# Performance work log

Measured on AMD Instinct MI355X. Metric: run time of the kernel, lower is better.

## Reference

```python
import jax, jax.numpy as jnp
import numpy as np

VERTEX_W = 1.0
SMOOTH_W = 0.1
SYM_W = 0.05
CHAMFER_W = 0.1

B, N = 4, 8192  # N points per cloud, flat dim = N*3


def setup_inputs() -> dict:
    key = jax.random.key(0)
    k1, k2 = jax.random.split(key)
    pred = jax.random.normal(k1, (B, N * 3), dtype=jnp.float32)
    targ = jax.random.normal(k2, (B, N * 3), dtype=jnp.float32)
    return {"pred_vertices": pred, "target_vertices": targ}


def _chamfer(x, y):
    # x: [B,N,3], y: [B,M,3]; euclidean cdist via matmul expansion
    x2 = jnp.sum(x * x, axis=-1)  # [B,N]
    y2 = jnp.sum(y * y, axis=-1)  # [B,M]
    xy = jnp.einsum('bnd,bmd->bnm', x, y)  # [B,N,M]
    d2 = x2[:, :, None] + y2[None if False else slice(None), None, :] - 2.0 * xy
    d = jnp.sqrt(jnp.maximum(d2, 0.0))
    return jnp.mean(jnp.min(d, axis=2)) + jnp.mean(jnp.min(d, axis=1))


def reference(pred_vertices, target_vertices):
    b = pred_vertices.shape[0]
    pv = pred_vertices.reshape(b, -1, 3)
    tv = target_vertices.reshape(b, -1, 3)

    # vertex MSE (on flat tensors, same as mse on reshaped)
    vertex_loss = jnp.mean((pred_vertices - target_vertices) ** 2)

    # smoothness: mean L2 norm of consecutive vertex diffs
    diff = pv[:, 1:, :] - pv[:, :-1, :]
    smoothness_loss = jnp.mean(jnp.linalg.norm(diff, axis=2))

    # symmetry: N is even in this config
    mid = pv.shape[1] // 2
    left = pv[:, :mid, :]
    right = jnp.flip(pv[:, mid:, :], axis=1)
    right = right.at[:, :, 0].multiply(-1.0)
    symmetry_loss = jnp.mean((left - right) ** 2)

    chamfer_loss = _chamfer(pv, tv)

    total = (VERTEX_W * vertex_loss + SMOOTH_W * smoothness_loss
             + SYM_W * symmetry_loss + CHAMFER_W * chamfer_loss)
    return total
```

## Files before the change

kernel.cpp:

```cpp
#include <hip/hip_runtime.h>
#include <hip/hip_bf16.h>


#define B_ 4
#define N_ 8192
#define MID_ (N_ / 2)
#define CNT_OFF 1536
#define RP_OFF 1664
#define PM_OFF 4096
#define PMC_OFF (PM_OFF + 8 * B_ * N_)
#define PACK_OFF (PMC_OFF + 16 * B_ * N_)
#define PACK_STRIDE (B_ * N_ * 16)

typedef short short8 __attribute__((ext_vector_type(8)));
typedef float f32x16 __attribute__((ext_vector_type(16)));

__global__ void AdvancedLoss3D_1881195675843_kernel() {}

__device__ __forceinline__ void async16(void* lds, const void* g) {
    __builtin_amdgcn_global_load_lds(
        (const __attribute__((address_space(1))) unsigned int*)g,
        (__attribute__((address_space(3))) unsigned int*)lds,
        16, 0, 0);
}

__device__ inline unsigned short bfu(float x) {
    union { __hip_bfloat16 b; unsigned short u; } c;
    c.b = __float2bfloat16(x);
    return c.u;
}
__device__ inline float bff(unsigned short u) {
    union { __hip_bfloat16 b; unsigned short u; } c;
    c.u = u;
    return __bfloat162float(c.b);
}

__device__ __forceinline__ float min3f(float a, float b, float c) {
    return fminf(fminf(a, b), c);
}
__device__ __forceinline__ float tree16(f32x16 v) {
    float m0 = min3f(v[0],  v[1],  v[2]);
    float m1 = min3f(v[3],  v[4],  v[5]);
    float m2 = min3f(v[6],  v[7],  v[8]);
    float m3 = min3f(v[9],  v[10], v[11]);
    float m4 = min3f(v[12], v[13], v[14]);
    return fminf(min3f(m0, m1, m2), min3f(m3, m4, v[15]));
}

__device__ inline void encA(float x, float y, float z, unsigned short* A) {
    float n2 = fmaf(x, x, fmaf(y, y, z * z));
    unsigned short hx = bfu(x), hy = bfu(y), hz = bfu(z);
    float fx = bff(hx), fy = bff(hy), fz = bff(hz);
    unsigned short lx = bfu(x - fx), ly = bfu(y - fy), lz = bfu(z - fz);
    unsigned short mx = bfu(-2.f * fx), my = bfu(-2.f * fy), mz = bfu(-2.f * fz);
    unsigned short nx = bfu(-2.f * bff(lx)), ny = bfu(-2.f * bff(ly)),
                   nz = bfu(-2.f * bff(lz));
    unsigned short n2h = bfu(n2);
    unsigned short n2l = bfu(n2 - bff(n2h));
    unsigned short one = bfu(1.0f);
    A[0] = mx; A[1] = my; A[2] = mz;
    A[3] = mx; A[4] = my; A[5] = mz;
    A[6] = nx; A[7] = ny; A[8] = nz;
    A[9] = n2h; A[10] = n2l; A[11] = one; A[12] = one;
    A[13] = A[14] = A[15] = 0;
}
__device__ inline void encB(float x, float y, float z, unsigned short* Bv) {
    float n2 = fmaf(x, x, fmaf(y, y, z * z));
    unsigned short hx = bfu(x), hy = bfu(y), hz = bfu(z);
    float fx = bff(hx), fy = bff(hy), fz = bff(hz);
    unsigned short lx = bfu(x - fx), ly = bfu(y - fy), lz = bfu(z - fz);
    unsigned short n2h = bfu(n2);
    unsigned short n2l = bfu(n2 - bff(n2h));
    unsigned short one = bfu(1.0f);
    Bv[0] = hx; Bv[1] = hy; Bv[2] = hz;
    Bv[3] = lx; Bv[4] = ly; Bv[5] = lz;
    Bv[6] = hx; Bv[7] = hy; Bv[8] = hz;
    Bv[9] = one; Bv[10] = one; Bv[11] = n2h; Bv[12] = n2l;
    Bv[13] = Bv[14] = Bv[15] = 0;
}

__global__ __launch_bounds__(64) void prep_aux(const float* __restrict__ pred,
                                               const float* __restrict__ targ,
                                               float* __restrict__ ws) {
    int idx = blockIdx.x * 64 + threadIdx.x;
    int b = idx >> 13;
    int i = idx & (N_ - 1);
    const float* p = pred + (size_t)idx * 3;
    const float* t = targ + (size_t)idx * 3;
    float px = p[0], py = p[1], pz = p[2];
    float tx = t[0], ty = t[1], tz = t[2];

    if (idx == 0) ((unsigned int*)ws)[CNT_OFF] = 0u;

    unsigned short* pk = (unsigned short*)(ws + PACK_OFF);
    {
        union U { unsigned short s[16]; uint4 q[2]; } ua, ud;
        encA(px, py, pz, ua.s);
        encB(tx, ty, tz, ud.s);
        uint4* ap = (uint4*)(pk + (size_t)idx * 16);
        ap[0] = ua.q[0]; ap[1] = ua.q[1];
        uint4* bt = (uint4*)(pk + PACK_STRIDE + (size_t)idx * 16);
        bt[0] = ud.q[0]; bt[1] = ud.q[1];
    }

    float dx = px - tx, dy = py - ty, dz = pz - tz;
    float dv = dx * dx + dy * dy + dz * dz;

    float sm = 0.f;
    if (i < N_ - 1) {
        float ex = p[3] - px, ey = p[4] - py, ez = p[5] - pz;
        sm = sqrtf(ex * ex + ey * ey + ez * ez);
    }

    float sy = 0.f;
    if (i < MID_) {
        const float* r = pred + ((size_t)(b * N_ + (N_ - 1 - i))) * 3;
        float ax = px + r[0];
        float ay = py - r[1];
        float az = pz - r[2];
        sy = ax * ax + ay * ay + az * az;
    }

    for (int off = 32; off; off >>= 1) {
        dv += __shfl_down(dv, off, 64);
        sm += __shfl_down(sm, off, 64);
        sy += __shfl_down(sy, off, 64);
    }
    if (threadIdx.x == 0) {
        ws[3 * blockIdx.x + 0] = dv;
        ws[3 * blockIdx.x + 1] = sm;
        ws[3 * blockIdx.x + 2] = sy;
    }
}

__global__ __launch_bounds__(256, 2) void chamfer_mfma(const unsigned short* __restrict__ packs,
                                                       float* __restrict__ ws) {
    int bid = blockIdx.x;
    int chunk = bid & 31;
    int rgb = bid >> 5;
    int b   = chunk >> 3;
    int cc  = chunk & 7;
    int w   = threadIdx.x >> 6;
    int l   = threadIdx.x & 63;
    int lr  = l & 31;
    int kh  = l >> 5;

    const unsigned short* Ap = packs;
    const unsigned short* Bp = packs + PACK_STRIDE;

    int rowbase = (rgb * 4 + w) * 128;
    const unsigned short* abase = Ap + ((size_t)(b * N_ + rowbase + lr)) * 16 + kh * 8;
    short8 af[4];
#pragma unroll
    for (int i = 0; i < 4; i++)
        af[i] = *(const short8*)(abase + i * 32 * 16);

    float rmin[4][16];
#pragma unroll
    for (int i = 0; i < 4; i++)
#pragma unroll
        for (int j = 0; j < 16; j++) rmin[i][j] = 3.4e38f;

    __shared__ __align__(16) unsigned char smem[65536];
    float (*colbuf)[1024] = (float (*)[1024])(smem + 32768);

    const unsigned short* bchunk = Bp + (size_t)(b * N_ + cc * 1024) * 16;
    {
        const unsigned short* src = bchunk + (size_t)(lr * 16 + kh * 8);
#pragma unroll
        for (int t = 0; t < 8; t++) {
            int tile = w * 8 + t;
            async16(smem + (size_t)tile * 1024, src + (size_t)tile * 512);
        }
    }
    __syncthreads();

    const f32x16 zero = {0.f, 0.f, 0.f, 0.f, 0.f, 0.f, 0.f, 0.f,
                         0.f, 0.f, 0.f, 0.f, 0.f, 0.f, 0.f, 0.f};
    const unsigned char* bl = smem + kh * 512 + lr * 16;
    for (int t = 0; t < 32; t += 2) {
        short8 bE = *(const short8*)(bl + (size_t)t * 1024);
        short8 bO = *(const short8*)(bl + (size_t)(t + 1) * 1024);
        float cmE = 3.4e38f, cmO = 3.4e38f;
#pragma unroll
        for (int i = 0; i < 4; i++) {
            f32x16 aE = __builtin_amdgcn_mfma_f32_32x32x16_bf16(af[i], bE, zero, 0, 0, 0);
            f32x16 aO = __builtin_amdgcn_mfma_f32_32x32x16_bf16(af[i], bO, zero, 0, 0, 0);
#pragma unroll
            for (int j = 0; j < 16; j++)
                rmin[i][j] = min3f(rmin[i][j], aE[j], aO[j]);
            cmE = fminf(cmE, tree16(aE));
            cmO = fminf(cmO, tree16(aO));
        }
        cmE = fminf(cmE, __shfl_xor(cmE, 32, 64));
        cmO = fminf(cmO, __shfl_xor(cmO, 32, 64));
        colbuf[w][t * 32 + lr] = cmE;
        colbuf[w][(t + 1) * 32 + lr] = cmO;
    }
    __syncthreads();

    {
        float* pmc = ws + PMC_OFF + (size_t)rgb * 32768 + b * N_ + cc * 1024;
#pragma unroll
        for (int c0 = 0; c0 < 1024; c0 += 256) {
            int c = c0 + threadIdx.x;
            pmc[c] = fminf(fminf(colbuf[0][c], colbuf[1][c]),
                           fminf(colbuf[2][c], colbuf[3][c]));
        }
    }
    __syncthreads();

    float (*sred)[128][32] = (float (*)[128][32])smem;
#pragma unroll
    for (int i = 0; i < 4; i++)
#pragma unroll
        for (int j = 0; j < 16; j++) {
            int r = i * 32 + (j & 3) + 8 * (j >> 2) + 4 * kh;
            sred[w][r][(lr + r) & 31] = rmin[i][j];
        }
    __syncthreads();
    float* orow = ws + PM_OFF + (size_t)cc * 32768 + b * N_ + rowbase;
#pragma unroll
    for (int rr = 0; rr < 128; rr += 64) {
        int r = rr + l;
        float v = 3.4e38f;
#pragma unroll
        for (int c = 0; c < 32; c++)
            v = fminf(v, sred[w][r][(c + r) & 31]);
        orow[r] = v;
    }
}

__global__ __launch_bounds__(256) void reduce_compose(const float* __restrict__ ws_ro,
                                                      float* __restrict__ ws,
                                                      unsigned int* __restrict__ out) {
    int bid = blockIdx.x, tid = threadIdx.x;
    int idx = bid * 256 + tid;
    float v = 3.4e38f;
    if (idx < B_ * N_) {
        const float* pmr = ws_ro + PM_OFF;
#pragma unroll
        for (int s = 0; s < 8; s++)
            v = fminf(v, pmr[(size_t)s * 32768 + idx]);
    } else {
        int c = idx - B_ * N_;
        const float* pmc = ws_ro + PMC_OFF;
#pragma unroll
        for (int s = 0; s < 16; s++)
            v = fminf(v, pmc[(size_t)s * 32768 + c]);
    }
    float d = sqrtf(fmaxf(v, 0.f));
    for (int off = 32; off; off >>= 1) d += __shfl_down(d, off, 64);
    __shared__ float red[4];
    __shared__ int is_last;
    int lane = tid & 63, w = tid >> 6;
    if (lane == 0) red[w] = d;
    __syncthreads();
    if (tid == 0) {
        ws[RP_OFF + bid] = red[0] + red[1] + red[2] + red[3];
        __threadfence();
        unsigned old = atomicAdd((unsigned int*)ws + CNT_OFF, 1u);
        is_last = (old == 255u);
    }
    __syncthreads();
    if (!is_last) return;

    if (tid == 0) __threadfence();
    __syncthreads();
    float rp = ws[RP_OFF + tid];
    float cr = (tid < 128) ? rp : 0.f;
    float cc = (tid < 128) ? 0.f : rp;
    float dv = ws[3 * tid]     + ws[3 * (tid + 256)];
    float sm = ws[3 * tid + 1] + ws[3 * (tid + 256) + 1];
    float sy = ws[3 * tid + 2] + ws[3 * (tid + 256) + 2];
    for (int off = 32; off; off >>= 1) {
        dv += __shfl_down(dv, off, 64);
        sm += __shfl_down(sm, off, 64);
        sy += __shfl_down(sy, off, 64);
        cr += __shfl_down(cr, off, 64);
        cc += __shfl_down(cc, off, 64);
    }
    __shared__ float red5[5][4];
    if (lane == 0) { red5[0][w] = dv; red5[1][w] = sm; red5[2][w] = sy;
                     red5[3][w] = cr; red5[4][w] = cc; }
    __syncthreads();
    if (tid == 0) {
        float S[5];
#pragma unroll
        for (int q = 0; q < 5; q++)
            S[q] = red5[q][0] + red5[q][1] + red5[q][2] + red5[q][3];
        float vertex = S[0] / (float)(B_ * N_ * 3);
        float smooth = S[1] / (float)(B_ * (N_ - 1));
        float sym    = S[2] / (float)(B_ * MID_ * 3);
        float cham   = (S[3] + S[4]) / (float)(B_ * N_);
        float total  = vertex + 0.1f * smooth + 0.05f * sym + 0.1f * cham;
        union { __hip_bfloat16 b; unsigned short u; } cv;
        cv.b = __float2bfloat16(total);
        out[0] = ((unsigned int)cv.u << 16) | (unsigned int)cv.u;
    }
}

extern "C" void kernel_launch(void* const* d_in, const int* in_sizes, int n_in,
                              void* d_out, int out_size, void* d_ws, size_t ws_size,
                              hipStream_t stream) {
    (void)in_sizes; (void)n_in; (void)out_size; (void)ws_size;
    const float* pred = (const float*)d_in[0];
    const float* targ = (const float*)d_in[1];
    float* wsf = (float*)d_ws;

    prep_aux<<<dim3(512), dim3(64), 0, stream>>>(pred, targ, wsf);
    chamfer_mfma<<<dim3(512), dim3(256), 0, stream>>>(
        (const unsigned short*)(wsf + PACK_OFF), wsf);
    reduce_compose<<<dim3(256), dim3(256), 0, stream>>>(
        wsf, wsf, (unsigned int*)d_out);
}
```

Before: 83.20 us.

## Fuse bf16 encoding into chamfer kernel and move aux losses into reduction

Result: faster. 79.16 us, median of 2 (-4.8%).

```diff
diff --git a/kernel.cpp b/kernel.cpp
--- a/kernel.cpp
+++ b/kernel.cpp
@@ -9,20 +9,11 @@
 #define RP_OFF 1664
 #define PM_OFF 4096
 #define PMC_OFF (PM_OFF + 8 * B_ * N_)
-#define PACK_OFF (PMC_OFF + 16 * B_ * N_)
-#define PACK_STRIDE (B_ * N_ * 16)
 
 typedef short short8 __attribute__((ext_vector_type(8)));
 typedef float f32x16 __attribute__((ext_vector_type(16)));
 
 __global__ void AdvancedLoss3D_1881195675843_kernel() {}
-
-__device__ __forceinline__ void async16(void* lds, const void* g) {
-    __builtin_amdgcn_global_load_lds(
-        (const __attribute__((address_space(1))) unsigned int*)g,
-        (__attribute__((address_space(3))) unsigned int*)lds,
-        16, 0, 0);
-}
 
 __device__ inline unsigned short bfu(float x) {
     union { __hip_bfloat16 b; unsigned short u; } c;
@@ -47,7 +38,7 @@
     return fminf(min3f(m0, m1, m2), min3f(m3, m4, v[15]));
 }
 
-__device__ inline void encA(float x, float y, float z, unsigned short* A) {
+__device__ __forceinline__ short8 encA_half(float x, float y, float z, int kh) {
     float n2 = fmaf(x, x, fmaf(y, y, z * z));
     unsigned short hx = bfu(x), hy = bfu(y), hz = bfu(z);
     float fx = bff(hx), fy = bff(hy), fz = bff(hz);
@@ -58,13 +49,14 @@
     unsigned short n2h = bfu(n2);
     unsigned short n2l = bfu(n2 - bff(n2h));
     unsigned short one = bfu(1.0f);
-    A[0] = mx; A[1] = my; A[2] = mz;
-    A[3] = mx; A[4] = my; A[5] = mz;
-    A[6] = nx; A[7] = ny; A[8] = nz;
-    A[9] = n2h; A[10] = n2l; A[11] = one; A[12] = one;
-    A[13] = A[14] = A[15] = 0;
-}
-__device__ inline void encB(float x, float y, float z, unsigned short* Bv) {
+    short8 lo = {(short)mx, (short)my, (short)mz, (short)mx,
+                 (short)my, (short)mz, (short)nx, (short)ny};
+    short8 hi = {(short)nz, (short)n2h, (short)n2l, (short)one,
+                 (short)one, 0, 0, 0};
+    return kh ? hi : lo;
+}
+__device__ __forceinline__ void encB(float x, float y, float z,
+                                     unsigned short* Bv) {
     float n2 = fmaf(x, x, fmaf(y, y, z * z));
     unsigned short hx = bfu(x), hy = bfu(y), hz = bfu(z);
     float fx = bff(hx), fy = bff(hy), fz = bff(hz);
@@ -79,100 +71,55 @@
     Bv[13] = Bv[14] = Bv[15] = 0;
 }
 
-__global__ __launch_bounds__(64) void prep_aux(const float* __restrict__ pred,
-                                               const float* __restrict__ targ,
-                                               float* __restrict__ ws) {
-    int idx = blockIdx.x * 64 + threadIdx.x;
-    int b = idx >> 13;
-    int i = idx & (N_ - 1);
-    const float* p = pred + (size_t)idx * 3;
-    const float* t = targ + (size_t)idx * 3;
-    float px = p[0], py = p[1], pz = p[2];
-    float tx = t[0], ty = t[1], tz = t[2];
-
-    if (idx == 0) ((unsigned int*)ws)[CNT_OFF] = 0u;
-
-    unsigned short* pk = (unsigned short*)(ws + PACK_OFF);
-    {
-        union U { unsigned short s[16]; uint4 q[2]; } ua, ud;
-        encA(px, py, pz, ua.s);
-        encB(tx, ty, tz, ud.s);
-        uint4* ap = (uint4*)(pk + (size_t)idx * 16);
-        ap[0] = ua.q[0]; ap[1] = ua.q[1];
-        uint4* bt = (uint4*)(pk + PACK_STRIDE + (size_t)idx * 16);
-        bt[0] = ud.q[0]; bt[1] = ud.q[1];
-    }
-
-    float dx = px - tx, dy = py - ty, dz = pz - tz;
-    float dv = dx * dx + dy * dy + dz * dz;
-
-    float sm = 0.f;
-    if (i < N_ - 1) {
-        float ex = p[3] - px, ey = p[4] - py, ez = p[5] - pz;
-        sm = sqrtf(ex * ex + ey * ey + ez * ez);
-    }
-
-    float sy = 0.f;
-    if (i < MID_) {
-        const float* r = pred + ((size_t)(b * N_ + (N_ - 1 - i))) * 3;
-        float ax = px + r[0];
-        float ay = py - r[1];
-        float az = pz - r[2];
-        sy = ax * ax + ay * ay + az * az;
-    }
-
-    for (int off = 32; off; off >>= 1) {
-        dv += __shfl_down(dv, off, 64);
-        sm += __shfl_down(sm, off, 64);
-        sy += __shfl_down(sy, off, 64);
-    }
-    if (threadIdx.x == 0) {
-        ws[3 * blockIdx.x + 0] = dv;
-        ws[3 * blockIdx.x + 1] = sm;
-        ws[3 * blockIdx.x + 2] = sy;
-    }
-}
-
-__global__ __launch_bounds__(256, 2) void chamfer_mfma(const unsigned short* __restrict__ packs,
+__global__ __launch_bounds__(256, 2) void chamfer_mfma(const float* __restrict__ pred,
+                                                       const float* __restrict__ targ,
                                                        float* __restrict__ ws) {
     int bid = blockIdx.x;
     int chunk = bid & 31;
     int rgb = bid >> 5;
     int b   = chunk >> 3;
     int cc  = chunk & 7;
-    int w   = threadIdx.x >> 6;
-    int l   = threadIdx.x & 63;
+    int tid = threadIdx.x;
+    int w   = tid >> 6;
+    int l   = tid & 63;
     int lr  = l & 31;
     int kh  = l >> 5;
 
-    const unsigned short* Ap = packs;
-    const unsigned short* Bp = packs + PACK_STRIDE;
-
-    int rowbase = (rgb * 4 + w) * 128;
-    const unsigned short* abase = Ap + ((size_t)(b * N_ + rowbase + lr)) * 16 + kh * 8;
-    short8 af[4];
-#pragma unroll
-    for (int i = 0; i < 4; i++)
-        af[i] = *(const short8*)(abase + i * 32 * 16);
-
-    float rmin[4][16];
-#pragma unroll
-    for (int i = 0; i < 4; i++)
-#pragma unroll
-        for (int j = 0; j < 16; j++) rmin[i][j] = 3.4e38f;
+    if (bid == 0 && tid == 0)
+        ((unsigned int*)ws)[CNT_OFF] = 0u;
 
     __shared__ __align__(16) unsigned char smem[65536];
     float (*colbuf)[1024] = (float (*)[1024])(smem + 32768);
 
-    const unsigned short* bchunk = Bp + (size_t)(b * N_ + cc * 1024) * 16;
     {
-        const unsigned short* src = bchunk + (size_t)(lr * 16 + kh * 8);
-#pragma unroll
-        for (int t = 0; t < 8; t++) {
-            int tile = w * 8 + t;
-            async16(smem + (size_t)tile * 1024, src + (size_t)tile * 512);
-        }
-    }
+        const float* tb = targ + (size_t)(b * N_ + cc * 1024) * 3;
+#pragma unroll
+        for (int j = 0; j < 4; j++) {
+            int c = tid + 256 * j;
+            float x = tb[3 * c], y = tb[3 * c + 1], z = tb[3 * c + 2];
+            union { unsigned short s[16]; uint4 q[2]; } e;
+            encB(x, y, z, e.s);
+            unsigned char* base = smem + (size_t)(c >> 5) * 1024 + (c & 31) * 16;
+            *(uint4*)(base)       = e.q[0];
+            *(uint4*)(base + 512) = e.q[1];
+        }
+    }
+
+    int rowbase = (rgb * 4 + w) * 128;
+    short8 af[4];
+    {
+        const float* pb = pred + (size_t)(b * N_ + rowbase + lr) * 3;
+#pragma unroll
+        for (int i = 0; i < 4; i++)
+            af[i] = encA_half(pb[i * 96], pb[i * 96 + 1], pb[i * 96 + 2], kh);
+    }
+
+    float rmin[4][16];
+#pragma unroll
+    for (int i = 0; i < 4; i++)
+#pragma unroll
+        for (int j = 0; j < 16; j++) rmin[i][j] = 3.4e38f;
+
     __syncthreads();
 
     const f32x16 zero = {0.f, 0.f, 0.f, 0.f, 0.f, 0.f, 0.f, 0.f,
@@ -203,7 +150,7 @@
         float* pmc = ws + PMC_OFF + (size_t)rgb * 32768 + b * N_ + cc * 1024;
 #pragma unroll
         for (int c0 = 0; c0 < 1024; c0 += 256) {
-            int c = c0 + threadIdx.x;
+            int c = c0 + tid;
             pmc[c] = fminf(fminf(colbuf[0][c], colbuf[1][c]),
                            fminf(colbuf[2][c], colbuf[3][c]));
         }
@@ -231,33 +178,63 @@
     }
 }
 
-__global__ __launch_bounds__(256) void reduce_compose(const float* __restrict__ ws_ro,
+__global__ __launch_bounds__(256) void reduce_compose(const float* __restrict__ pred,
+                                                      const float* __restrict__ targ,
                                                       float* __restrict__ ws,
                                                       unsigned int* __restrict__ out) {
     int bid = blockIdx.x, tid = threadIdx.x;
     int idx = bid * 256 + tid;
     float v = 3.4e38f;
+    float dv = 0.f, sm = 0.f, sy = 0.f;
     if (idx < B_ * N_) {
-        const float* pmr = ws_ro + PM_OFF;
+        const float* pmr = ws + PM_OFF;
 #pragma unroll
         for (int s = 0; s < 8; s++)
             v = fminf(v, pmr[(size_t)s * 32768 + idx]);
+
+        int b = idx >> 13;
+        int i = idx & (N_ - 1);
+        const float* p = pred + (size_t)idx * 3;
+        const float* t = targ + (size_t)idx * 3;
+        float px = p[0], py = p[1], pz = p[2];
+        float tx = t[0], ty = t[1], tz = t[2];
+        float dx = px - tx, dy = py - ty, dz = pz - tz;
+        dv = dx * dx + dy * dy + dz * dz;
+        if (i < N_ - 1) {
+            float ex = p[3] - px, ey = p[4] - py, ez = p[5] - pz;
+            sm = sqrtf(ex * ex + ey * ey + ez * ez);
+        }
+        if (i < MID_) {
+            const float* r = pred + ((size_t)(b * N_ + (N_ - 1 - i))) * 3;
+            float ax = px + r[0];
+            float ay = py - r[1];
+            float az = pz - r[2];
+            sy = ax * ax + ay * ay + az * az;
+        }
     } else {
         int c = idx - B_ * N_;
-        const float* pmc = ws_ro + PMC_OFF;
+        const float* pmc = ws + PMC_OFF;
 #pragma unroll
         for (int s = 0; s < 16; s++)
             v = fminf(v, pmc[(size_t)s * 32768 + c]);
     }
     float d = sqrtf(fmaxf(v, 0.f));
-    for (int off = 32; off; off >>= 1) d += __shfl_down(d, off, 64);
-    __shared__ float red[4];
+    for (int off = 32; off; off >>= 1) {
+        d  += __shfl_down(d, off, 64);
+        dv += __shfl_down(dv, off, 64);
+        sm += __shfl_down(sm, off, 64);
+        sy += __shfl_down(sy, off, 64);
+    }
+    __shared__ float red[4][4];
     __shared__ int is_last;
     int lane = tid & 63, w = tid >> 6;
-    if (lane == 0) red[w] = d;
+    if (lane == 0) { red[0][w] = d; red[1][w] = dv; red[2][w] = sm; red[3][w] = sy; }
     __syncthreads();
     if (tid == 0) {
-        ws[RP_OFF + bid] = red[0] + red[1] + red[2] + red[3];
+        ws[RP_OFF + bid] = red[0][0] + red[0][1] + red[0][2] + red[0][3];
+        ws[3 * bid + 0]  = red[1][0] + red[1][1] + red[1][2] + red[1][3];
+        ws[3 * bid + 1]  = red[2][0] + red[2][1] + red[2][2] + red[2][3];
+        ws[3 * bid + 2]  = red[3][0] + red[3][1] + red[3][2] + red[3][3];
         __threadfence();
         unsigned old = atomicAdd((unsigned int*)ws + CNT_OFF, 1u);
         is_last = (old == 255u);
@@ -270,19 +247,17 @@
     float rp = ws[RP_OFF + tid];
     float cr = (tid < 128) ? rp : 0.f;
     float cc = (tid < 128) ? 0.f : rp;
-    float dv = ws[3 * tid]     + ws[3 * (tid + 256)];
-    float sm = ws[3 * tid + 1] + ws[3 * (tid + 256) + 1];
-    float sy = ws[3 * tid + 2] + ws[3 * (tid + 256) + 2];
+    float dvs = ws[3 * tid], sms = ws[3 * tid + 1], sys = ws[3 * tid + 2];
     for (int off = 32; off; off >>= 1) {
-        dv += __shfl_down(dv, off, 64);
-        sm += __shfl_down(sm, off, 64);
-        sy += __shfl_down(sy, off, 64);
-        cr += __shfl_down(cr, off, 64);
-        cc += __shfl_down(cc, off, 64);
+        dvs += __shfl_down(dvs, off, 64);
+        sms += __shfl_down(sms, off, 64);
+        sys += __shfl_down(sys, off, 64);
+        cr  += __shfl_down(cr, off, 64);
+        cc  += __shfl_down(cc, off, 64);
     }
     __shared__ float red5[5][4];
-    if (lane == 0) { red5[0][w] = dv; red5[1][w] = sm; red5[2][w] = sy;
-                     red5[3][w] = cr; red5[4][w] = cc; }
+    if (lane == 0) { red5[0][w] = dvs; red5[1][w] = sms; red5[2][w] = sys;
+                     red5[3][w] = cr;  red5[4][w] = cc; }
     __syncthreads();
     if (tid == 0) {
         float S[5];
@@ -308,9 +283,7 @@
     const float* targ = (const float*)d_in[1];
     float* wsf = (float*)d_ws;
 
-    prep_aux<<<dim3(512), dim3(64), 0, stream>>>(pred, targ, wsf);
-    chamfer_mfma<<<dim3(512), dim3(256), 0, stream>>>(
-        (const unsigned short*)(wsf + PACK_OFF), wsf);
+    chamfer_mfma<<<dim3(512), dim3(256), 0, stream>>>(pred, targ, wsf);
     reduce_compose<<<dim3(256), dim3(256), 0, stream>>>(
-        wsf, wsf, (unsigned int*)d_out);
-}
+        pred, targ, wsf, (unsigned int*)d_out);
+}
```
